# Optimization experiments

Hardware: AMD Instinct MI355X
Metric: run time of the kernel (lower is better)

The kernel has to match this reference:

```python
import jax, jax.numpy as jnp
import numpy as np

B, T, D, K = 16, 4096, 256, 1024

def setup_inputs() -> dict:
    key = jax.random.key(0)
    k1, k2 = jax.random.split(key)
    inputs = jax.random.normal(k1, (B, T, D), dtype=jnp.float32)
    codebook = jax.random.normal(k2, (K, D), dtype=jnp.float32)
    return {"inputs": inputs, "codebook": codebook}

def reference(inputs, codebook):
    # argmin over squared distance == argmin over L2 distance (cdist p=2).
    x2 = jnp.sum(inputs * inputs, axis=-1, keepdims=True)          # [B,T,1]
    c2 = jnp.sum(codebook * codebook, axis=-1)                      # [K]
    xc = jnp.einsum('btd,kd->btk', inputs, codebook)                # [B,T,K]
    d2 = x2 + c2[None, None, :] - 2.0 * xc                          # [B,T,K]
    assignment = jnp.argmin(d2, axis=-1)                            # [B,T]
    quantized = codebook[assignment]                                # [B,T,D]
    # Straight-through estimator
    out = jax.lax.stop_gradient(quantized - inputs) + inputs
    return out
```

## Files before the change

### kernel.cpp

```cpp
#include <hip/hip_runtime.h>
#include <float.h>


typedef _Float16 f16;
typedef f16 f16x8 __attribute__((ext_vector_type(8)));
typedef f16 f16x4 __attribute__((ext_vector_type(4)));
typedef float f32x4 __attribute__((ext_vector_type(4)));

#define DDIM    256
#define KCODES  1024
#define NTOK    65536
#define SMARGIN 0.1f

#define ASW(r, cbyte) ((r) * 128 + ((cbyte) ^ (((r) & 7) << 4)))

__global__ __launch_bounds__(256) void vq_prep(const float* __restrict__ cb,
                                               f16* __restrict__ ch,
                                               float* __restrict__ c2,
                                               unsigned* __restrict__ count) {
    const int k    = blockIdx.x * 4 + (threadIdx.x >> 6);
    const int lane = threadIdx.x & 63;
    const float4 v = *(const float4*)(cb + (size_t)k * DDIM + 4 * lane);
    f16x4 h; h[0] = (f16)v.x; h[1] = (f16)v.y; h[2] = (f16)v.z; h[3] = (f16)v.w;
    *(f16x4*)(ch + (size_t)k * DDIM + 4 * lane) = h;
    float s = v.x * v.x + v.y * v.y + v.z * v.z + v.w * v.w;
    #pragma unroll
    for (int off = 32; off > 0; off >>= 1) s += __shfl_down(s, off, 64);
    if (lane == 0) c2[k] = s;
    if (blockIdx.x == 0 && threadIdx.x == 0) *count = 0u;
}

__global__ __launch_bounds__(256, 2) void vq_main(const float* __restrict__ xg,
                                                  const f16* __restrict__ ch,
                                                  const float* __restrict__ c2,
                                                  const float* __restrict__ cb,
                                                  float* __restrict__ out,
                                                  unsigned* __restrict__ count,
                                                  unsigned* __restrict__ list) {
    __shared__ f16   As[2 * 8192];
    __shared__ float c2s[KCODES];
    __shared__ float wmv[2][128];
    __shared__ int   wmi[2][128];
    __shared__ float wms[2][128];
    __shared__ float runv[128], runs[128];
    __shared__ int   runi[128];
    __shared__ int   idx_s[128];

    const int t    = threadIdx.x;
    const int wave = t >> 6, lane = t & 63;
    const int wm   = wave >> 1;
    const int tn   = wave & 1;
    const int q    = lane >> 4;
    const int m16  = lane & 15;
    const int tok0 = blockIdx.x * 128;
    const int swz  = (m16 & 7) << 4;
    const int srow = t >> 3;
    const int sc16 = t & 7;

    f16x8 bfrag[4][8];
    #pragma unroll
    for (int ti = 0; ti < 4; ++ti) {
        const size_t row = (size_t)(tok0 + tn * 64 + ti * 16 + m16) * DDIM;
        #pragma unroll
        for (int ks = 0; ks < 8; ++ks) {
            const float* p = xg + row + ks * 32 + q * 8;
            const float4 u0 = *(const float4*)(p);
            const float4 u1 = *(const float4*)(p + 4);
            f16x8 b;
            b[0] = (f16)u0.x; b[1] = (f16)u0.y; b[2] = (f16)u0.z; b[3] = (f16)u0.w;
            b[4] = (f16)u1.x; b[5] = (f16)u1.y; b[6] = (f16)u1.z; b[7] = (f16)u1.w;
            bfrag[ti][ks] = b;
        }
    }

    *(float4*)&c2s[t * 4] = *(const float4*)(c2 + t * 4);
    if (t < 128) { runv[t] = -FLT_MAX; runs[t] = -FLT_MAX; runi[t] = 0; }

    f16x8 sreg[4];
    #pragma unroll
    for (int i = 0; i < 4; ++i)
        sreg[i] = *(const f16x8*)(ch + (size_t)(srow + 32 * i) * DDIM + sc16 * 8);
    __syncthreads();

    for (int nc = 0; nc < 8; ++nc) {
        f32x4 acc[4][4];
        #pragma unroll
        for (int ci = 0; ci < 4; ++ci) {
            f32x4 cv = *(const f32x4*)&c2s[nc * 128 + wm * 64 + ci * 16 + q * 4];
            cv = cv * -0.5f;
            #pragma unroll
            for (int ti = 0; ti < 4; ++ti) acc[ci][ti] = cv;
        }

        #pragma unroll
        for (int st = 0; st < 4; ++st) {
            char* Ab = (char*)As + (st & 1) * 16384;
            #pragma unroll
            for (int i = 0; i < 4; ++i) {
                const int r = srow + 32 * i;
                *(f16x8*)(Ab + ASW(r, sc16 * 16)) = sreg[i];
            }
            if (!(nc == 7 && st == 3)) {
                const int nn = nc + (st == 3 ? 1 : 0);
                const int ns = (st + 1) & 3;
                #pragma unroll
                for (int i = 0; i < 4; ++i)
                    sreg[i] = *(const f16x8*)(ch + (size_t)(nn * 128 + srow + 32 * i) * DDIM
                                              + ns * 64 + sc16 * 8);
            }
            __syncthreads();

            const char* Ar = (const char*)As + (st & 1) * 16384;
            const int rbase = (wm * 64 + m16) * 128;
            #pragma unroll
            for (int kk = 0; kk < 2; ++kk) {
                const int col = ((kk << 6) | (q << 4)) ^ swz;
                f16x8 af[4];
                #pragma unroll
                for (int ci = 0; ci < 4; ++ci)
                    af[ci] = *(const f16x8*)(Ar + rbase + ci * 2048 + col);
                #pragma unroll
                for (int ci = 0; ci < 4; ++ci)
                    #pragma unroll
                    for (int ti = 0; ti < 4; ++ti)
                        acc[ci][ti] = __builtin_amdgcn_mfma_f32_16x16x32_f16(
                            af[ci], bfrag[ti][st * 2 + kk], acc[ci][ti], 0, 0, 0);
            }

            if (st == 3) {
                const int kbase = nc * 128 + wm * 64;
                #pragma unroll
                for (int ti = 0; ti < 4; ++ti) {
                    float b1 = -FLT_MAX, b2 = -FLT_MAX; int i1 = 0;
                    #pragma unroll
                    for (int ci = 0; ci < 4; ++ci) {
                        #pragma unroll
                        for (int r = 0; r < 4; ++r) {
                            const float v = acc[ci][ti][r];
                            const int   c = kbase + ci * 16 + q * 4 + r;
                            const bool gt = v > b1;
                            b2 = fmaxf(b2, gt ? b1 : v);
                            i1 = gt ? c : i1;
                            b1 = gt ? v : b1;
                        }
                    }
                    #pragma unroll
                    for (int sft = 0; sft < 2; ++sft) {
                        const int off = 16 << sft;
                        const float ob1 = __shfl_xor(b1, off, 64);
                        const float ob2 = __shfl_xor(b2, off, 64);
                        const int   oi1 = __shfl_xor(i1, off, 64);
                        const bool better = (ob1 > b1) || (ob1 == b1 && oi1 < i1);
                        b2 = fmaxf(fmaxf(b2, ob2), fminf(b1, ob1));
                        b1 = better ? ob1 : b1;
                        i1 = better ? oi1 : i1;
                    }
                    if (lane < 16) {
                        const int tl = tn * 64 + ti * 16 + m16;
                        wmv[wm][tl] = b1; wmi[wm][tl] = i1; wms[wm][tl] = b2;
                    }
                }
                __syncthreads();
                if (t < 128) {
                    const float a1 = wmv[0][t], a2 = wms[0][t];
                    const int   ai = wmi[0][t];
                    const float b1_ = wmv[1][t], b2_ = wms[1][t];
                    const int   bi_ = wmi[1][t];
                    const bool bb = (b1_ > a1) || (b1_ == a1 && bi_ < ai);
                    const float c1 = bb ? b1_ : a1;
                    const int   ci_ = bb ? bi_ : ai;
                    const float cs = fmaxf(fmaxf(a2, b2_), fminf(a1, b1_));
                    const float r1 = runv[t];
                    runs[t] = fmaxf(fmaxf(runs[t], cs), fminf(r1, c1));
                    if (c1 > r1) { runv[t] = c1; runi[t] = ci_; }
                }
            }
        }
    }

    __syncthreads();
    if (t < 128) {
        idx_s[t] = runi[t];
        if (runv[t] - runs[t] < SMARGIN) {
            const unsigned p = atomicAdd(count, 1u);
            list[p] = tok0 + t;
        }
    }
    __syncthreads();

    #pragma unroll
    for (int i = 0; i < 32; ++i) {
        const int f   = i * 256 + t;
        const int tok = f >> 6, d4 = f & 63;
        const int code = idx_s[tok];
        const float4 v = *(const float4*)(cb + (size_t)code * DDIM + 4 * d4);
        *(float4*)(out + (size_t)(tok0 + tok) * DDIM + 4 * d4) = v;
    }
}

__global__ __launch_bounds__(256) void vq_rescue(const float* __restrict__ xg,
                                                 const float* __restrict__ cb,
                                                 const float* __restrict__ c2,
                                                 const unsigned* __restrict__ count,
                                                 const unsigned* __restrict__ list,
                                                 float* __restrict__ out) {
    __shared__ float xls[8][DDIM];
    __shared__ float rv[4][8];
    __shared__ int   ri[4][8];
    __shared__ int   bidx[8];

    const int t = threadIdx.x;
    const int wave = t >> 6, lane = t & 63;
    const unsigned n = *count;

    for (unsigned base = blockIdx.x * 8; base < n; base += gridDim.x * 8) {
        const int nb = (int)min(8u, n - base);
        __syncthreads();
        #pragma unroll
        for (int i = 0; i < 2; ++i) {
            const int f = t + 256 * i;
            const int row = f >> 6, d4 = f & 63;
            if (row < nb)
                *(float4*)&xls[row][4 * d4] =
                    *(const float4*)(xg + (size_t)list[base + row] * DDIM + 4 * d4);
        }
        __syncthreads();

        float acc[4][8];
        #pragma unroll
        for (int j = 0; j < 4; ++j)
            #pragma unroll
            for (int tk = 0; tk < 8; ++tk) acc[j][tk] = 0.0f;

        for (int d4 = 0; d4 < 64; ++d4) {
            float4 cv[4];
            #pragma unroll
            for (int j = 0; j < 4; ++j)
                cv[j] = *(const float4*)(cb + (size_t)(4 * t + j) * DDIM + 4 * d4);
            #pragma unroll
            for (int tk = 0; tk < 8; ++tk) {
                const float4 xv = *(const float4*)&xls[tk][4 * d4];
                #pragma unroll
                for (int j = 0; j < 4; ++j) {
                    float a = acc[j][tk];
                    a = fmaf(cv[j].x, xv.x, a);
                    a = fmaf(cv[j].y, xv.y, a);
                    a = fmaf(cv[j].z, xv.z, a);
                    a = fmaf(cv[j].w, xv.w, a);
                    acc[j][tk] = a;
                }
            }
        }

        #pragma unroll
        for (int tk = 0; tk < 8; ++tk) {
            if (tk < nb) {
                float b1 = FLT_MAX; int i1 = 0;
                #pragma unroll
                for (int j = 0; j < 4; ++j) {
                    const float d = fmaf(-2.0f, acc[j][tk], c2[4 * t + j]);
                    if (d < b1) { b1 = d; i1 = 4 * t + j; }
                }
                #pragma unroll
                for (int off = 32; off > 0; off >>= 1) {
                    const float ov = __shfl_xor(b1, off, 64);
                    const int   oi = __shfl_xor(i1, off, 64);
                    if (ov < b1 || (ov == b1 && oi < i1)) { b1 = ov; i1 = oi; }
                }
                if (lane == 0) { rv[wave][tk] = b1; ri[wave][tk] = i1; }
            }
        }
        __syncthreads();
        if (t < 8 && t < nb) {
            float bv = rv[0][t]; int bi = ri[0][t];
            #pragma unroll
            for (int w = 1; w < 4; ++w)
                if (rv[w][t] < bv || (rv[w][t] == bv && ri[w][t] < bi)) {
                    bv = rv[w][t]; bi = ri[w][t];
                }
            bidx[t] = bi;
        }
        __syncthreads();

        #pragma unroll
        for (int i = 0; i < 2; ++i) {
            const int f = t + 256 * i;
            const int row = f >> 6, d4 = f & 63;
            if (row < nb) {
                const int code = bidx[row];
                const float4 v = *(const float4*)(cb + (size_t)code * DDIM + 4 * d4);
                *(float4*)(out + (size_t)list[base + row] * DDIM + 4 * d4) = v;
            }
        }
    }
}

extern "C" void kernel_launch(void* const* d_in, const int* in_sizes, int n_in,
                              void* d_out, int out_size, void* d_ws, size_t ws_size,
                              hipStream_t stream) {
    const float* x  = (const float*)d_in[0];
    const float* cb = (const float*)d_in[1];
    float* out = (float*)d_out;

    char* ws = (char*)d_ws;
    f16*      ch    = (f16*)ws;
    float*    c2    = (float*)(ws + 524288);
    unsigned* count = (unsigned*)(ws + 528448);
    unsigned* list  = (unsigned*)(ws + 528512);

    hipLaunchKernelGGL(vq_prep,   dim3(KCODES / 4), dim3(256), 0, stream, cb, ch, c2, count);
    hipLaunchKernelGGL(vq_main,   dim3(NTOK / 128), dim3(256), 0, stream,
                       x, ch, c2, cb, out, count, list);
    hipLaunchKernelGGL(vq_rescue, dim3(1024),       dim3(256), 0, stream,
                       x, cb, c2, count, list, out);
}
```

Baseline: 227.8 us.

## Pre-swizzle codebook into MFMA fragment layout and read it directly from global

The prep kernel now writes the f16 codebook in a tiled layout that matches the MFMA A-fragment, so each lane loads its fragment straight from global (L2-cached) memory. The shared-memory staging, double buffer and per-stage barriers are gone from the main loop. Per-chunk argmin state now stays in registers per wave, with one cross-wave merge at the end, which removes the per-chunk shared-memory reduction and its syncs. The trade-off is that every wave reloads codebook fragments from global/L2 instead of sharing them through LDS, which adds global traffic and load latency to the MFMA loop.

```diff
diff --git a/kernel.cpp b/kernel.cpp
--- a/kernel.cpp
+++ b/kernel.cpp
@@ -12,38 +12,39 @@
 #define NTOK    65536
 #define SMARGIN 0.1f
 
-#define ASW(r, cbyte) ((r) * 128 + ((cbyte) ^ (((r) & 7) << 4)))
-
 __global__ __launch_bounds__(256) void vq_prep(const float* __restrict__ cb,
-                                               f16* __restrict__ ch,
+                                               f16* __restrict__ cht,
                                                float* __restrict__ c2,
                                                unsigned* __restrict__ count) {
     const int k    = blockIdx.x * 4 + (threadIdx.x >> 6);
     const int lane = threadIdx.x & 63;
     const float4 v = *(const float4*)(cb + (size_t)k * DDIM + 4 * lane);
     f16x4 h; h[0] = (f16)v.x; h[1] = (f16)v.y; h[2] = (f16)v.z; h[3] = (f16)v.w;
-    *(f16x4*)(ch + (size_t)k * DDIM + 4 * lane) = h;
-    float s = v.x * v.x + v.y * v.y + v.z * v.z + v.w * v.w;
-    #pragma unroll
-    for (int off = 32; off > 0; off >>= 1) s += __shfl_down(s, off, 64);
-    if (lane == 0) c2[k] = s;
+    const int ct = k >> 4, m = k & 15;
+    const int e  = 4 * lane;
+    const int kt = e >> 5;
+    const int s  = (e & 31) >> 3;
+    const int j0 = e & 7;
+    const int L  = s * 16 + m;
+    *(f16x4*)(cht + ((size_t)(ct * 8 + kt) * 64 + L) * 8 + j0) = h;
+    float ssum = v.x * v.x + v.y * v.y + v.z * v.z + v.w * v.w;
+    #pragma unroll
+    for (int off = 32; off > 0; off >>= 1) ssum += __shfl_down(ssum, off, 64);
+    if (lane == 0) c2[k] = ssum;
     if (blockIdx.x == 0 && threadIdx.x == 0) *count = 0u;
 }
 
 __global__ __launch_bounds__(256, 2) void vq_main(const float* __restrict__ xg,
-                                                  const f16* __restrict__ ch,
+                                                  const f16* __restrict__ cht,
                                                   const float* __restrict__ c2,
                                                   const float* __restrict__ cb,
                                                   float* __restrict__ out,
                                                   unsigned* __restrict__ count,
                                                   unsigned* __restrict__ list) {
-    __shared__ f16   As[2 * 8192];
     __shared__ float c2s[KCODES];
     __shared__ float wmv[2][128];
     __shared__ int   wmi[2][128];
     __shared__ float wms[2][128];
-    __shared__ float runv[128], runs[128];
-    __shared__ int   runi[128];
     __shared__ int   idx_s[128];
 
     const int t    = threadIdx.x;
@@ -53,9 +54,6 @@
     const int q    = lane >> 4;
     const int m16  = lane & 15;
     const int tok0 = blockIdx.x * 128;
-    const int swz  = (m16 & 7) << 4;
-    const int srow = t >> 3;
-    const int sc16 = t & 7;
 
     f16x8 bfrag[4][8];
     #pragma unroll
@@ -74,14 +72,15 @@
     }
 
     *(float4*)&c2s[t * 4] = *(const float4*)(c2 + t * 4);
-    if (t < 128) { runv[t] = -FLT_MAX; runs[t] = -FLT_MAX; runi[t] = 0; }
-
-    f16x8 sreg[4];
-    #pragma unroll
-    for (int i = 0; i < 4; ++i)
-        sreg[i] = *(const f16x8*)(ch + (size_t)(srow + 32 * i) * DDIM + sc16 * 8);
     __syncthreads();
 
+    float rb1[4], rb2[4]; int ri1[4];
+    #pragma unroll
+    for (int ti = 0; ti < 4; ++ti) { rb1[ti] = -FLT_MAX; rb2[ti] = -FLT_MAX; ri1[ti] = 0; }
+
+    const f16* aw = cht + wm * 16384 + lane * 8;
+
+    #pragma unroll 1
     for (int nc = 0; nc < 8; ++nc) {
         f32x4 acc[4][4];
         #pragma unroll
@@ -92,96 +91,72 @@
             for (int ti = 0; ti < 4; ++ti) acc[ci][ti] = cv;
         }
 
-        #pragma unroll
-        for (int st = 0; st < 4; ++st) {
-            char* Ab = (char*)As + (st & 1) * 16384;
-            #pragma unroll
-            for (int i = 0; i < 4; ++i) {
-                const int r = srow + 32 * i;
-                *(f16x8*)(Ab + ASW(r, sc16 * 16)) = sreg[i];
-            }
-            if (!(nc == 7 && st == 3)) {
-                const int nn = nc + (st == 3 ? 1 : 0);
-                const int ns = (st + 1) & 3;
-                #pragma unroll
-                for (int i = 0; i < 4; ++i)
-                    sreg[i] = *(const f16x8*)(ch + (size_t)(nn * 128 + srow + 32 * i) * DDIM
-                                              + ns * 64 + sc16 * 8);
-            }
-            __syncthreads();
-
-            const char* Ar = (const char*)As + (st & 1) * 16384;
-            const int rbase = (wm * 64 + m16) * 128;
-            #pragma unroll
-            for (int kk = 0; kk < 2; ++kk) {
-                const int col = ((kk << 6) | (q << 4)) ^ swz;
-                f16x8 af[4];
-                #pragma unroll
-                for (int ci = 0; ci < 4; ++ci)
-                    af[ci] = *(const f16x8*)(Ar + rbase + ci * 2048 + col);
-                #pragma unroll
-                for (int ci = 0; ci < 4; ++ci)
-                    #pragma unroll
-                    for (int ti = 0; ti < 4; ++ti)
-                        acc[ci][ti] = __builtin_amdgcn_mfma_f32_16x16x32_f16(
-                            af[ci], bfrag[ti][st * 2 + kk], acc[ci][ti], 0, 0, 0);
-            }
-
-            if (st == 3) {
-                const int kbase = nc * 128 + wm * 64;
-                #pragma unroll
-                for (int ti = 0; ti < 4; ++ti) {
-                    float b1 = -FLT_MAX, b2 = -FLT_MAX; int i1 = 0;
-                    #pragma unroll
-                    for (int ci = 0; ci < 4; ++ci) {
-                        #pragma unroll
-                        for (int r = 0; r < 4; ++r) {
-                            const float v = acc[ci][ti][r];
-                            const int   c = kbase + ci * 16 + q * 4 + r;
-                            const bool gt = v > b1;
-                            b2 = fmaxf(b2, gt ? b1 : v);
-                            i1 = gt ? c : i1;
-                            b1 = gt ? v : b1;
-                        }
-                    }
-                    #pragma unroll
-                    for (int sft = 0; sft < 2; ++sft) {
-                        const int off = 16 << sft;
-                        const float ob1 = __shfl_xor(b1, off, 64);
-                        const float ob2 = __shfl_xor(b2, off, 64);
-                        const int   oi1 = __shfl_xor(i1, off, 64);
-                        const bool better = (ob1 > b1) || (ob1 == b1 && oi1 < i1);
-                        b2 = fmaxf(fmaxf(b2, ob2), fminf(b1, ob1));
-                        b1 = better ? ob1 : b1;
-                        i1 = better ? oi1 : i1;
-                    }
-                    if (lane < 16) {
-                        const int tl = tn * 64 + ti * 16 + m16;
-                        wmv[wm][tl] = b1; wmi[wm][tl] = i1; wms[wm][tl] = b2;
-                    }
-                }
-                __syncthreads();
-                if (t < 128) {
-                    const float a1 = wmv[0][t], a2 = wms[0][t];
-                    const int   ai = wmi[0][t];
-                    const float b1_ = wmv[1][t], b2_ = wms[1][t];
-                    const int   bi_ = wmi[1][t];
-                    const bool bb = (b1_ > a1) || (b1_ == a1 && bi_ < ai);
-                    const float c1 = bb ? b1_ : a1;
-                    const int   ci_ = bb ? bi_ : ai;
-                    const float cs = fmaxf(fmaxf(a2, b2_), fminf(a1, b1_));
-                    const float r1 = runv[t];
-                    runs[t] = fmaxf(fmaxf(runs[t], cs), fminf(r1, c1));
-                    if (c1 > r1) { runv[t] = c1; runi[t] = ci_; }
-                }
-            }
-        }
-    }
-
+        const f16* an = aw + nc * 32768;
+        #pragma unroll
+        for (int ks = 0; ks < 8; ++ks) {
+            f16x8 af[4];
+            #pragma unroll
+            for (int ci = 0; ci < 4; ++ci)
+                af[ci] = *(const f16x8*)(an + ci * 4096 + ks * 512);
+            #pragma unroll
+            for (int ci = 0; ci < 4; ++ci)
+                #pragma unroll
+                for (int ti = 0; ti < 4; ++ti)
+                    acc[ci][ti] = __builtin_amdgcn_mfma_f32_16x16x32_f16(
+                        af[ci], bfrag[ti][ks], acc[ci][ti], 0, 0, 0);
+        }
+
+        const int kbase = nc * 128 + wm * 64;
+        #pragma unroll
+        for (int ti = 0; ti < 4; ++ti) {
+            float b1 = -FLT_MAX, b2 = -FLT_MAX; int i1 = 0;
+            #pragma unroll
+            for (int ci = 0; ci < 4; ++ci) {
+                #pragma unroll
+                for (int r = 0; r < 4; ++r) {
+                    const float v = acc[ci][ti][r];
+                    const int   c = kbase + ci * 16 + q * 4 + r;
+                    const bool gt = v > b1;
+                    b2 = fmaxf(b2, gt ? b1 : v);
+                    i1 = gt ? c : i1;
+                    b1 = gt ? v : b1;
+                }
+            }
+            #pragma unroll
+            for (int sft = 0; sft < 2; ++sft) {
+                const int off = 16 << sft;
+                const float ob1 = __shfl_xor(b1, off, 64);
+                const float ob2 = __shfl_xor(b2, off, 64);
+                const int   oi1 = __shfl_xor(i1, off, 64);
+                const bool better = (ob1 > b1) || (ob1 == b1 && oi1 < i1);
+                b2 = fmaxf(fmaxf(b2, ob2), fminf(b1, ob1));
+                b1 = better ? ob1 : b1;
+                i1 = better ? oi1 : i1;
+            }
+            rb2[ti] = fmaxf(fmaxf(rb2[ti], b2), fminf(rb1[ti], b1));
+            if (b1 > rb1[ti]) { rb1[ti] = b1; ri1[ti] = i1; }
+        }
+    }
+
+    #pragma unroll
+    for (int ti = 0; ti < 4; ++ti) {
+        if (lane < 16) {
+            const int tl = tn * 64 + ti * 16 + m16;
+            wmv[wm][tl] = rb1[ti]; wmi[wm][tl] = ri1[ti]; wms[wm][tl] = rb2[ti];
+        }
+    }
     __syncthreads();
     if (t < 128) {
-        idx_s[t] = runi[t];
-        if (runv[t] - runs[t] < SMARGIN) {
+        const float a1 = wmv[0][t], a2 = wms[0][t];
+        const int   ai = wmi[0][t];
+        const float b1_ = wmv[1][t], b2_ = wms[1][t];
+        const int   bi_ = wmi[1][t];
+        const bool bb = (b1_ > a1) || (b1_ == a1 && bi_ < ai);
+        const float c1 = bb ? b1_ : a1;
+        const int   ci_ = bb ? bi_ : ai;
+        const float cs = fmaxf(fmaxf(a2, b2_), fminf(a1, b1_));
+        idx_s[t] = ci_;
+        if (c1 - cs < SMARGIN) {
             const unsigned p = atomicAdd(count, 1u);
             list[p] = tok0 + t;
         }
@@ -303,14 +278,14 @@
     float* out = (float*)d_out;
 
     char* ws = (char*)d_ws;
-    f16*      ch    = (f16*)ws;
+    f16*      cht   = (f16*)ws;
     float*    c2    = (float*)(ws + 524288);
     unsigned* count = (unsigned*)(ws + 528448);
     unsigned* list  = (unsigned*)(ws + 528512);
 
-    hipLaunchKernelGGL(vq_prep,   dim3(KCODES / 4), dim3(256), 0, stream, cb, ch, c2, count);
+    hipLaunchKernelGGL(vq_prep,   dim3(KCODES / 4), dim3(256), 0, stream, cb, cht, c2, count);
     hipLaunchKernelGGL(vq_main,   dim3(NTOK / 128), dim3(256), 0, stream,
-                       x, ch, c2, cb, out, count, list);
+                       x, cht, c2, cb, out, count, list);
     hipLaunchKernelGGL(vq_rescue, dim3(1024),       dim3(256), 0, stream,
                        x, cb, c2, count, list, out);
 }
```

After: 257.1 us. 1.13x slower.

## Give each wave a private codebook LDS tile and drop block barriers

Applied to the files above, without the earlier changes.

Each wave now stages only the 64 codebook rows it consumes into its own LDS region, so the per-stage __syncthreads barriers and the per-chunk cross-wave merge are removed. Running best and second-best values are kept in registers per wave and merged across the two code halves once at the end. MFMA sections are wrapped in s_setprio to favour matrix issue. The trade-off is that the two waves sharing a code half (wm) each load and stage the same rows, doubling global loads of the f16 codebook and adding register pressure (8 staging registers instead of 4). There is also no intra-wave ordering guaranteed between the LDS writes and the following reads.

```diff
diff --git a/kernel.cpp b/kernel.cpp
--- a/kernel.cpp
+++ b/kernel.cpp
@@ -11,8 +11,6 @@
 #define KCODES  1024
 #define NTOK    65536
 #define SMARGIN 0.1f
-
-#define ASW(r, cbyte) ((r) * 128 + ((cbyte) ^ (((r) & 7) << 4)))
 
 __global__ __launch_bounds__(256) void vq_prep(const float* __restrict__ cb,
                                                f16* __restrict__ ch,
@@ -37,13 +35,11 @@
                                                   float* __restrict__ out,
                                                   unsigned* __restrict__ count,
                                                   unsigned* __restrict__ list) {
-    __shared__ f16   As[2 * 8192];
+    __shared__ f16   As[4 * 4096];
     __shared__ float c2s[KCODES];
     __shared__ float wmv[2][128];
     __shared__ int   wmi[2][128];
     __shared__ float wms[2][128];
-    __shared__ float runv[128], runs[128];
-    __shared__ int   runi[128];
     __shared__ int   idx_s[128];
 
     const int t    = threadIdx.x;
@@ -54,8 +50,9 @@
     const int m16  = lane & 15;
     const int tok0 = blockIdx.x * 128;
     const int swz  = (m16 & 7) << 4;
-    const int srow = t >> 3;
-    const int sc16 = t & 7;
+    const int wswz = ((lane & 7) ^ (lane >> 3)) << 4;
+    const int r0   = lane >> 3;
+    const int g0   = (lane & 7) * 8;
 
     f16x8 bfrag[4][8];
     #pragma unroll
@@ -74,13 +71,19 @@
     }
 
     *(float4*)&c2s[t * 4] = *(const float4*)(c2 + t * 4);
-    if (t < 128) { runv[t] = -FLT_MAX; runs[t] = -FLT_MAX; runi[t] = 0; }
-
-    f16x8 sreg[4];
-    #pragma unroll
-    for (int i = 0; i < 4; ++i)
-        sreg[i] = *(const f16x8*)(ch + (size_t)(srow + 32 * i) * DDIM + sc16 * 8);
+
+    f16x8 sreg[8];
+    #pragma unroll
+    for (int i = 0; i < 8; ++i)
+        sreg[i] = *(const f16x8*)(ch + (size_t)(wm * 64 + r0 + 8 * i) * DDIM + g0);
+
     __syncthreads();
+
+    float rb1[4], rb2[4]; int ri1[4];
+    #pragma unroll
+    for (int ti = 0; ti < 4; ++ti) { rb1[ti] = -FLT_MAX; rb2[ti] = -FLT_MAX; ri1[ti] = 0; }
+
+    char* wb = (char*)As + wave * 8192;
 
     for (int nc = 0; nc < 8; ++nc) {
         f32x4 acc[4][4];
@@ -94,31 +97,25 @@
 
         #pragma unroll
         for (int st = 0; st < 4; ++st) {
-            char* Ab = (char*)As + (st & 1) * 16384;
-            #pragma unroll
-            for (int i = 0; i < 4; ++i) {
-                const int r = srow + 32 * i;
-                *(f16x8*)(Ab + ASW(r, sc16 * 16)) = sreg[i];
-            }
+            #pragma unroll
+            for (int i = 0; i < 8; ++i)
+                *(f16x8*)(wb + (r0 + 8 * i) * 128 + wswz) = sreg[i];
             if (!(nc == 7 && st == 3)) {
                 const int nn = nc + (st == 3 ? 1 : 0);
                 const int ns = (st + 1) & 3;
                 #pragma unroll
-                for (int i = 0; i < 4; ++i)
-                    sreg[i] = *(const f16x8*)(ch + (size_t)(nn * 128 + srow + 32 * i) * DDIM
-                                              + ns * 64 + sc16 * 8);
-            }
-            __syncthreads();
-
-            const char* Ar = (const char*)As + (st & 1) * 16384;
-            const int rbase = (wm * 64 + m16) * 128;
+                for (int i = 0; i < 8; ++i)
+                    sreg[i] = *(const f16x8*)(ch + (size_t)(nn * 128 + wm * 64 + r0 + 8 * i) * DDIM
+                                              + ns * 64 + g0);
+            }
+            __builtin_amdgcn_s_setprio(1);
             #pragma unroll
             for (int kk = 0; kk < 2; ++kk) {
                 const int col = ((kk << 6) | (q << 4)) ^ swz;
                 f16x8 af[4];
                 #pragma unroll
                 for (int ci = 0; ci < 4; ++ci)
-                    af[ci] = *(const f16x8*)(Ar + rbase + ci * 2048 + col);
+                    af[ci] = *(const f16x8*)(wb + (ci * 16 + m16) * 128 + col);
                 #pragma unroll
                 for (int ci = 0; ci < 4; ++ci)
                     #pragma unroll
@@ -126,62 +123,60 @@
                         acc[ci][ti] = __builtin_amdgcn_mfma_f32_16x16x32_f16(
                             af[ci], bfrag[ti][st * 2 + kk], acc[ci][ti], 0, 0, 0);
             }
-
-            if (st == 3) {
-                const int kbase = nc * 128 + wm * 64;
-                #pragma unroll
-                for (int ti = 0; ti < 4; ++ti) {
-                    float b1 = -FLT_MAX, b2 = -FLT_MAX; int i1 = 0;
-                    #pragma unroll
-                    for (int ci = 0; ci < 4; ++ci) {
-                        #pragma unroll
-                        for (int r = 0; r < 4; ++r) {
-                            const float v = acc[ci][ti][r];
-                            const int   c = kbase + ci * 16 + q * 4 + r;
-                            const bool gt = v > b1;
-                            b2 = fmaxf(b2, gt ? b1 : v);
-                            i1 = gt ? c : i1;
-                            b1 = gt ? v : b1;
-                        }
-                    }
-                    #pragma unroll
-                    for (int sft = 0; sft < 2; ++sft) {
-                        const int off = 16 << sft;
-                        const float ob1 = __shfl_xor(b1, off, 64);
-                        const float ob2 = __shfl_xor(b2, off, 64);
-                        const int   oi1 = __shfl_xor(i1, off, 64);
-                        const bool better = (ob1 > b1) || (ob1 == b1 && oi1 < i1);
-                        b2 = fmaxf(fmaxf(b2, ob2), fminf(b1, ob1));
-                        b1 = better ? ob1 : b1;
-                        i1 = better ? oi1 : i1;
-                    }
-                    if (lane < 16) {
-                        const int tl = tn * 64 + ti * 16 + m16;
-                        wmv[wm][tl] = b1; wmi[wm][tl] = i1; wms[wm][tl] = b2;
-                    }
-                }
-                __syncthreads();
-                if (t < 128) {
-                    const float a1 = wmv[0][t], a2 = wms[0][t];
-                    const int   ai = wmi[0][t];
-                    const float b1_ = wmv[1][t], b2_ = wms[1][t];
-                    const int   bi_ = wmi[1][t];
-                    const bool bb = (b1_ > a1) || (b1_ == a1 && bi_ < ai);
-                    const float c1 = bb ? b1_ : a1;
-                    const int   ci_ = bb ? bi_ : ai;
-                    const float cs = fmaxf(fmaxf(a2, b2_), fminf(a1, b1_));
-                    const float r1 = runv[t];
-                    runs[t] = fmaxf(fmaxf(runs[t], cs), fminf(r1, c1));
-                    if (c1 > r1) { runv[t] = c1; runi[t] = ci_; }
-                }
-            }
-        }
-    }
-
+            __builtin_amdgcn_s_setprio(0);
+        }
+
+        const int kbase = nc * 128 + wm * 64;
+        #pragma unroll
+        for (int ti = 0; ti < 4; ++ti) {
+            float b1 = -FLT_MAX, b2 = -FLT_MAX; int i1 = 0;
+            #pragma unroll
+            for (int ci = 0; ci < 4; ++ci) {
+                #pragma unroll
+                for (int r = 0; r < 4; ++r) {
+                    const float v = acc[ci][ti][r];
+                    const int   c = kbase + ci * 16 + q * 4 + r;
+                    const bool gt = v > b1;
+                    b2 = fmaxf(b2, gt ? b1 : v);
+                    i1 = gt ? c : i1;
+                    b1 = gt ? v : b1;
+                }
+            }
+            #pragma unroll
+            for (int sft = 0; sft < 2; ++sft) {
+                const int off = 16 << sft;
+                const float ob1 = __shfl_xor(b1, off, 64);
+                const float ob2 = __shfl_xor(b2, off, 64);
+                const int   oi1 = __shfl_xor(i1, off, 64);
+                const bool better = (ob1 > b1) || (ob1 == b1 && oi1 < i1);
+                b2 = fmaxf(fmaxf(b2, ob2), fminf(b1, ob1));
+                b1 = better ? ob1 : b1;
+                i1 = better ? oi1 : i1;
+            }
+            rb2[ti] = fmaxf(fmaxf(rb2[ti], b2), fminf(rb1[ti], b1));
+            if (b1 > rb1[ti]) { rb1[ti] = b1; ri1[ti] = i1; }
+        }
+    }
+
+    #pragma unroll
+    for (int ti = 0; ti < 4; ++ti) {
+        if (lane < 16) {
+            const int tl = tn * 64 + ti * 16 + m16;
+            wmv[wm][tl] = rb1[ti]; wmi[wm][tl] = ri1[ti]; wms[wm][tl] = rb2[ti];
+        }
+    }
     __syncthreads();
     if (t < 128) {
-        idx_s[t] = runi[t];
-        if (runv[t] - runs[t] < SMARGIN) {
+        const float a1 = wmv[0][t], a2 = wms[0][t];
+        const int   ai = wmi[0][t];
+        const float b1_ = wmv[1][t], b2_ = wms[1][t];
+        const int   bi_ = wmi[1][t];
+        const bool bb = (b1_ > a1) || (b1_ == a1 && bi_ < ai);
+        const float c1 = bb ? b1_ : a1;
+        const int   ci_ = bb ? bi_ : ai;
+        const float cs = fmaxf(fmaxf(a2, b2_), fminf(a1, b1_));
+        idx_s[t] = ci_;
+        if (c1 - cs < SMARGIN) {
             const unsigned p = atomicAdd(count, 1u);
             list[p] = tok0 + t;
         }
```

New measurement: 232.1 us. Within noise of the previous version (+1.9%).
